# Performance work log

Measured on AMD Instinct MI355X. Metric: run time of the kernel, lower is better.

The kernel has to match this reference:

```python
import jax, jax.numpy as jnp
import numpy as np

N_NODES = 100000
N_EDGES = 1600000
N_FEAT = 128
HIDDEN = 128
N_CLASSES = 10
N_GRAPHS = 512


def setup_inputs() -> dict:
    key = jax.random.key(0)
    ks = jax.random.split(key, 20)

    def lin(k, fan_in, fan_out, bias=True):
        kw, kb = jax.random.split(k)
        s = 1.0 / np.sqrt(fan_in)
        W = jax.random.uniform(kw, (fan_in, fan_out), jnp.float32, -s, s)
        if bias:
            b = jax.random.uniform(kb, (fan_out,), jnp.float32, -s, s)
            return W, b
        return W

    x = jax.random.normal(ks[0], (N_NODES, N_FEAT), jnp.float32)
    edge_index = jax.random.randint(ks[1], (2, N_EDGES), 0, N_NODES)
    batch = jnp.sort(jax.random.randint(ks[2], (N_NODES,), 0, N_GRAPHS))

    w1l, b1 = lin(ks[3], N_FEAT, HIDDEN)
    w1r = lin(ks[4], N_FEAT, HIDDEN, bias=False)
    w2l, b2 = lin(ks[5], HIDDEN, HIDDEN)
    w2r = lin(ks[6], HIDDEN, HIDDEN, bias=False)
    w3l, b3 = lin(ks[7], HIDDEN, HIDDEN)
    w3r = lin(ks[8], HIDDEN, HIDDEN, bias=False)
    gate_w, gate_b = lin(ks[9], HIDDEN, 1)
    lin1_w, lin1_b = lin(ks[10], HIDDEN, HIDDEN)
    lin2_w, lin2_b = lin(ks[11], HIDDEN, N_CLASSES)

    return dict(x=x, edge_index=edge_index, batch=batch,
                w1l=w1l, b1=b1, w1r=w1r,
                w2l=w2l, b2=b2, w2r=w2r,
                w3l=w3l, b3=b3, w3r=w3r,
                gate_w=gate_w, gate_b=gate_b,
                lin1_w=lin1_w, lin1_b=lin1_b,
                lin2_w=lin2_w, lin2_b=lin2_b)


def _sage_conv(x, src, dst, Wl, bl, Wr, n_nodes):
    # PyG SAGEConv(mean): out = lin_l(mean_{j in N(i)} x_j) + lin_r(x_i)
    msg_sum = jax.ops.segment_sum(x[src], dst, num_segments=n_nodes)
    cnt = jax.ops.segment_sum(jnp.ones((src.shape[0], 1), x.dtype), dst,
                              num_segments=n_nodes)
    mean = msg_sum / jnp.maximum(cnt, 1.0)
    return mean @ Wl + bl + x @ Wr


def reference(x, edge_index, batch,
              w1l, b1, w1r, w2l, b2, w2r, w3l, b3, w3r,
              gate_w, gate_b, lin1_w, lin1_b, lin2_w, lin2_b):
    n = x.shape[0]
    src, dst = edge_index[0], edge_index[1]

    h = jax.nn.relu(_sage_conv(x, src, dst, w1l, b1, w1r, n))
    h = jax.nn.relu(_sage_conv(h, src, dst, w2l, b2, w2r, n))
    h = jax.nn.relu(_sage_conv(h, src, dst, w3l, b3, w3r, n))

    # AttentionalAggregation: scatter-softmax of gate over graph segments
    gate = h @ gate_w + gate_b                                  # [N, 1]
    m = jax.ops.segment_max(gate, batch, num_segments=N_GRAPHS)  # [G, 1]
    e = jnp.exp(gate - m[batch])
    s = jax.ops.segment_sum(e, batch, num_segments=N_GRAPHS)     # [G, 1]
    alpha = e / s[batch]
    pooled = jax.ops.segment_sum(alpha * h, batch, num_segments=N_GRAPHS)  # [G, H]

    out = jax.nn.relu(pooled @ lin1_w + lin1_b)
    # dropout is identity in eval mode
    out = out @ lin2_w + lin2_b
    return jax.nn.log_softmax(out, axis=-1)
```

## Files before the change

### kernel.cpp

```cpp
#include <hip/hip_runtime.h>
#include <stdint.h>

#define N_NODES 100000
#define N_EDGES 1600000
#define NF 128
#define NG 512
#define NC 10

#define NBUCK ((N_NODES + 255) / 256)
#define EPB 4096

#define KSTRIDE 136
#define GEMM_B ((N_NODES + 63) / 64)

#define CVT_B 6250
#define BT_B 384
#define BOUNDS_B 3
#define COUNT_B ((N_EDGES + EPB - 1) / EPB)

typedef short short8 __attribute__((ext_vector_type(8)));
typedef float f32x4 __attribute__((ext_vector_type(4)));

__device__ __forceinline__ unsigned short f2b(float f) {
    unsigned u = __float_as_uint(f);
    u += 0x7fffu + ((u >> 16) & 1u);
    return (unsigned short)(u >> 16);
}
__device__ __forceinline__ unsigned cvt2(float lo, float hi) {
    unsigned r;
    asm("v_cvt_pk_bf16_f32 %0, %1, %2" : "=v"(r) : "v"(lo), "v"(hi));
    return r;
}
__device__ __forceinline__ float lo16(unsigned v) { return __uint_as_float(v << 16); }
__device__ __forceinline__ float hi16(unsigned v) { return __uint_as_float(v & 0xffff0000u); }

__global__ __launch_bounds__(256) void prep_kernel(const float* __restrict__ x, unsigned short* __restrict__ xb,
                                                   const float* __restrict__ w1l, const float* __restrict__ w1r,
                                                   const float* __restrict__ w2l, const float* __restrict__ w2r,
                                                   const float* __restrict__ w3l, const float* __restrict__ w3r,
                                                   unsigned short* __restrict__ Bt,
                                                   const int* __restrict__ batch, int* __restrict__ gstart,
                                                   const int* __restrict__ dst, int* __restrict__ bcount) {
    const int b = blockIdx.x, t = threadIdx.x;
    if (b < CVT_B) {
        int i = b * 256 + t;
        const float4* ip = (const float4*)x;
        float4 a = ip[2 * i], c = ip[2 * i + 1];
        uint4 o;
        o.x = cvt2(a.x, a.y);
        o.y = cvt2(a.z, a.w);
        o.z = cvt2(c.x, c.y);
        o.w = cvt2(c.z, c.w);
        ((uint4*)xb)[i] = o;
    } else if (b < CVT_B + BT_B) {
        int i = (b - CVT_B) * 256 + t;
        int layer = i / (128 * 256);
        int r = i % (128 * 256);
        int n = r / 256, k = r % 256;
        const float* wl = (layer == 0) ? w1l : (layer == 1) ? w2l : w3l;
        const float* wr = (layer == 0) ? w1r : (layer == 1) ? w2r : w3r;
        float v = (k < 128) ? wl[k * 128 + n] : wr[(k - 128) * 128 + n];
        Bt[i] = f2b(v);
    } else if (b < CVT_B + BT_B + BOUNDS_B) {
        int g = (b - CVT_B - BT_B) * 256 + t;
        if (g > NG) return;
        int lo = 0, hi = N_NODES;
        while (lo < hi) {
            int mid = (lo + hi) >> 1;
            if (batch[mid] < g) lo = mid + 1; else hi = mid;
        }
        gstart[g] = lo;
    } else {
        __shared__ int h[NBUCK];
        for (int i = t; i < NBUCK; i += 256) h[i] = 0;
        __syncthreads();
        const int base = (b - CVT_B - BT_B - BOUNDS_B) * EPB;
        const int lim = min(base + EPB, N_EDGES);
        for (int i = base + t; i < lim; i += 256) atomicAdd(&h[dst[i] >> 8], 1);
        __syncthreads();
        for (int i = t; i < NBUCK; i += 256)
            if (h[i]) atomicAdd(&bcount[i], h[i]);
    }
}

__global__ __launch_bounds__(512) void bucket_scan(const int* __restrict__ bcount, int* __restrict__ bbase,
                                                   int* __restrict__ gcursor, int* __restrict__ rowptr) {
    __shared__ int sh[512];
    const int t = threadIdx.x;
    int v = (t < NBUCK) ? bcount[t] : 0;
    sh[t] = v;
    __syncthreads();
    for (int off = 1; off < 512; off <<= 1) {
        int u = (t >= off) ? sh[t - off] : 0;
        __syncthreads();
        sh[t] += u;
        __syncthreads();
    }
    if (t < NBUCK) {
        int e = sh[t] - v;
        bbase[t] = e;
        gcursor[t] = e;
    }
    if (t == NBUCK - 1) bbase[NBUCK] = sh[t];
    if (t == 0) rowptr[N_NODES] = N_EDGES;
}

__global__ __launch_bounds__(256) void bucket_scatter(const int* __restrict__ src, const int* __restrict__ dst,
                                                      int* __restrict__ gcursor, unsigned* __restrict__ brec) {
    __shared__ int h[NBUCK];
    for (int i = threadIdx.x; i < NBUCK; i += 256) h[i] = 0;
    __syncthreads();
    const int base = blockIdx.x * EPB;
    const int lim = min(base + EPB, N_EDGES);
    for (int i = base + threadIdx.x; i < lim; i += 256) atomicAdd(&h[dst[i] >> 8], 1);
    __syncthreads();
    for (int i = threadIdx.x; i < NBUCK; i += 256) {
        int c = h[i];
        if (c) h[i] = atomicAdd(&gcursor[i], c);
    }
    __syncthreads();
    for (int i = base + threadIdx.x; i < lim; i += 256) {
        int d = dst[i];
        int pos = atomicAdd(&h[d >> 8], 1);
        brec[pos] = ((unsigned)(d & 255) << 17) | (unsigned)src[i];
    }
}

__global__ __launch_bounds__(256) void bucket_fill(const unsigned* __restrict__ brec, const int* __restrict__ bbase,
                                                   int* __restrict__ rowptr, int* __restrict__ eidx) {
    __shared__ int nh[256];
    __shared__ int sc[256];
    const int b = blockIdx.x, t = threadIdx.x;
    const int beg = bbase[b], end = bbase[b + 1];
    nh[t] = 0;
    __syncthreads();
    for (int i = beg + t; i < end; i += 256) atomicAdd(&nh[brec[i] >> 17], 1);
    __syncthreads();
    int cnt = nh[t];
    sc[t] = cnt;
    __syncthreads();
    for (int off = 1; off < 256; off <<= 1) {
        int u = (t >= off) ? sc[t - off] : 0;
        __syncthreads();
        sc[t] += u;
        __syncthreads();
    }
    int excl = sc[t] - cnt;
    int node = b * 256 + t;
    if (node < N_NODES) rowptr[node] = beg + excl;
    nh[t] = beg + excl;
    __syncthreads();
    for (int i = beg + t; i < end; i += 256) {
        unsigned r = brec[i];
        int pos = atomicAdd(&nh[r >> 17], 1);
        eidx[pos] = (int)(r & 0x1FFFFu);
    }
}

__global__ __launch_bounds__(256) void agg_kernel(const unsigned short* __restrict__ F,
                                                  const int* __restrict__ rowptr,
                                                  const int* __restrict__ eidx,
                                                  unsigned short* __restrict__ M) {
    int node = blockIdx.x * 4 + (threadIdx.x >> 6);
    if (node >= N_NODES) return;
    const int lane = threadIdx.x & 63;
    const int quad = lane >> 4, ql = lane & 15;
    const int beg = rowptr[node], end = rowptr[node + 1];
    const char* Fb = (const char*)F;
    const unsigned qoff = (unsigned)ql << 4;

    float a0 = 0.f, a1 = 0.f, a2 = 0.f, a3 = 0.f, a4 = 0.f, a5 = 0.f, a6 = 0.f, a7 = 0.f;

    for (int cs = beg; cs < end; cs += 64) {
        int e = cs + lane;
        int idx = eidx[e < end ? e : end - 1];
        int n = end - cs;
        if (n > 64) n = 64;
        const int nfull = n >> 4;
        int l = quad;
        for (int g = 0; g < nfull; ++g, l += 16) {
            int r0 = __shfl(idx, l);
            int r1 = __shfl(idx, l + 4);
            int r2 = __shfl(idx, l + 8);
            int r3 = __shfl(idx, l + 12);
            uint4 v0 = *(const uint4*)(Fb + (((unsigned)r0 << 8) | qoff));
            uint4 v1 = *(const uint4*)(Fb + (((unsigned)r1 << 8) | qoff));
            uint4 v2 = *(const uint4*)(Fb + (((unsigned)r2 << 8) | qoff));
            uint4 v3 = *(const uint4*)(Fb + (((unsigned)r3 << 8) | qoff));
            a0 += lo16(v0.x) + lo16(v1.x) + lo16(v2.x) + lo16(v3.x);
            a1 += hi16(v0.x) + hi16(v1.x) + hi16(v2.x) + hi16(v3.x);
            a2 += lo16(v0.y) + lo16(v1.y) + lo16(v2.y) + lo16(v3.y);
            a3 += hi16(v0.y) + hi16(v1.y) + hi16(v2.y) + hi16(v3.y);
            a4 += lo16(v0.z) + lo16(v1.z) + lo16(v2.z) + lo16(v3.z);
            a5 += hi16(v0.z) + hi16(v1.z) + hi16(v2.z) + hi16(v3.z);
            a6 += lo16(v0.w) + lo16(v1.w) + lo16(v2.w) + lo16(v3.w);
            a7 += hi16(v0.w) + hi16(v1.w) + hi16(v2.w) + hi16(v3.w);
        }
        const int base = nfull << 4;
        for (int it = base; it < n; it += 4) {
            int l0 = it + quad;
            int r0 = __shfl(idx, l0 < n ? l0 : n - 1);
            float s0 = (l0 < n) ? 1.f : 0.f;
            uint4 v0 = *(const uint4*)(Fb + (((unsigned)r0 << 8) | qoff));
            a0 += s0 * lo16(v0.x); a1 += s0 * hi16(v0.x);
            a2 += s0 * lo16(v0.y); a3 += s0 * hi16(v0.y);
            a4 += s0 * lo16(v0.z); a5 += s0 * hi16(v0.z);
            a6 += s0 * lo16(v0.w); a7 += s0 * hi16(v0.w);
        }
    }

    a0 += __shfl_xor(a0, 16); a0 += __shfl_xor(a0, 32);
    a1 += __shfl_xor(a1, 16); a1 += __shfl_xor(a1, 32);
    a2 += __shfl_xor(a2, 16); a2 += __shfl_xor(a2, 32);
    a3 += __shfl_xor(a3, 16); a3 += __shfl_xor(a3, 32);
    a4 += __shfl_xor(a4, 16); a4 += __shfl_xor(a4, 32);
    a5 += __shfl_xor(a5, 16); a5 += __shfl_xor(a5, 32);
    a6 += __shfl_xor(a6, 16); a6 += __shfl_xor(a6, 32);
    a7 += __shfl_xor(a7, 16); a7 += __shfl_xor(a7, 32);

    if (quad == 0) {
        float inv = 1.0f / (float)max(end - beg, 1);
        uint4 o;
        o.x = cvt2(a0 * inv, a1 * inv);
        o.y = cvt2(a2 * inv, a3 * inv);
        o.z = cvt2(a4 * inv, a5 * inv);
        o.w = cvt2(a6 * inv, a7 * inv);
        ((uint4*)M)[(size_t)node * 16 + ql] = o;
    }
}

__global__ __launch_bounds__(256, 4) void gemm_kernel(const unsigned short* __restrict__ Am,
                                                      const unsigned short* __restrict__ Ax,
                                                      const unsigned short* __restrict__ Bt,
                                                      const float* __restrict__ bias,
                                                      unsigned short* __restrict__ Out,
                                                      const float* __restrict__ gatew,
                                                      const float* __restrict__ gateb,
                                                      float* __restrict__ gate) {
    const int t = threadIdx.x;
    const int wave = t >> 6, lane = t & 63;
    const int lrow = lane & 15, quad = lane >> 4;
    const int wrow0 = blockIdx.x * 64 + wave * 16;

    __shared__ __attribute__((aligned(16))) unsigned short Bs[128 * KSTRIDE];

    f32x4 acc[8];
#pragma unroll
    for (int j = 0; j < 8; ++j) acc[j] = (f32x4){0.f, 0.f, 0.f, 0.f};

    int arow = wrow0 + lrow;
    if (arow > N_NODES - 1) arow = N_NODES - 1;

    for (int p = 0; p < 2; ++p) {
        if (p) __syncthreads();
#pragma unroll
        for (int i = 0; i < 8; ++i) {
            int u = t + i * 256;
            int r = u >> 4, seg = u & 15;
            *(uint4*)(Bs + r * KSTRIDE + seg * 8) =
                *(const uint4*)(Bt + (size_t)r * 256 + p * 128 + seg * 8);
        }
        __syncthreads();

        const unsigned short* Aarr = p ? Ax : Am;
#pragma unroll
        for (int c = 0; c < 4; ++c) {
            const int kb = c * 32 + quad * 8;
            short8 af = *(const short8*)(Aarr + (size_t)arow * 128 + kb);
#pragma unroll
            for (int nt = 0; nt < 8; ++nt) {
                short8 bf = *(const short8*)(Bs + (nt * 16 + lrow) * KSTRIDE + kb);
                acc[nt] = __builtin_amdgcn_mfma_f32_16x16x32_bf16(af, bf, acc[nt], 0, 0, 0);
            }
        }
    }

    float gpart[4] = {0.f, 0.f, 0.f, 0.f};
    const int rbase = wrow0 + quad * 4;

#pragma unroll
    for (int nt = 0; nt < 8; ++nt) {
        int col = nt * 16 + lrow;
        float bc = bias[col];
        float gw = gatew ? gatew[col] : 0.f;
#pragma unroll
        for (int r = 0; r < 4; ++r) {
            int row = rbase + r;
            float v = fmaxf(acc[nt][r] + bc, 0.f);
            if (row < N_NODES) gpart[r] += v * gw;
            unsigned sv = (unsigned)f2b(v);
            unsigned nb = (unsigned)__shfl_xor((int)sv, 1);
            if (((lrow & 1) == 0) && row < N_NODES)
                *(unsigned*)(Out + (size_t)row * 128 + col) = sv | (nb << 16);
        }
    }
    if (gatew) {
        float gb = gateb[0];
#pragma unroll
        for (int r = 0; r < 4; ++r) {
            float g = gpart[r];
            g += __shfl_xor(g, 1);
            g += __shfl_xor(g, 2);
            g += __shfl_xor(g, 4);
            g += __shfl_xor(g, 8);
            if (lrow == 0) {
                int row = rbase + r;
                if (row < N_NODES) gate[row] = g + gb;
            }
        }
    }
}

__global__ __launch_bounds__(256) void pool_mlp_kernel(const unsigned short* __restrict__ h,
                                                       const float* __restrict__ gate,
                                                       const int* __restrict__ gstart,
                                                       const float* __restrict__ l1w,
                                                       const float* __restrict__ l1b,
                                                       const float* __restrict__ l2w,
                                                       const float* __restrict__ l2b,
                                                       float* __restrict__ out) {
    const int g = blockIdx.x;
    const int t = threadIdx.x;
    const int w = t >> 6, lane = t & 63;
    __shared__ float mred[4];
    __shared__ float sred[4];
    __shared__ float pax[4][128];
    __shared__ float pooled_s[128];
    __shared__ float hid_s[128];

    const int beg = gstart[g], end = gstart[g + 1];

    float m = -INFINITY;
    for (int i = beg + t; i < end; i += 256) m = fmaxf(m, gate[i]);
#pragma unroll
    for (int o = 32; o; o >>= 1) m = fmaxf(m, __shfl_xor(m, o));
    if (lane == 0) mred[w] = m;
    __syncthreads();
    m = fmaxf(fmaxf(mred[0], mred[1]), fmaxf(mred[2], mred[3]));

    float s = 0.f, ax = 0.f, ay = 0.f;
    const unsigned* hb = (const unsigned*)h;
    for (int i = beg + w; i < end; i += 4) {
        float e = expf(gate[i] - m);
        unsigned v = hb[(size_t)i * 64 + lane];
        s += e;
        ax += e * lo16(v);
        ay += e * hi16(v);
    }
    if (lane == 0) sred[w] = s;
    pax[w][2 * lane] = ax;
    pax[w][2 * lane + 1] = ay;
    __syncthreads();

    if (t < 128) {
        float ssum = sred[0] + sred[1] + sred[2] + sred[3];
        float invs = (ssum > 0.f) ? 1.0f / ssum : 0.f;
        pooled_s[t] = (pax[0][t] + pax[1][t] + pax[2][t] + pax[3][t]) * invs;
    }
    __syncthreads();

    if (w < 2) {
        const int o = w * 64 + lane;
        float acc = l1b[o];
        for (int k = 0; k < 128; ++k) acc += pooled_s[k] * l1w[k * 128 + o];
        hid_s[o] = fmaxf(acc, 0.f);
    }
    __syncthreads();

    if (w == 0) {
        float o10 = 0.f;
        if (lane < NC) {
            o10 = l2b[lane];
            for (int k = 0; k < 128; ++k) o10 += hid_s[k] * l2w[k * NC + lane];
        }
        float mm = -INFINITY;
#pragma unroll
        for (int j = 0; j < NC; ++j) mm = fmaxf(mm, __shfl(o10, j));
        float ss = 0.f;
#pragma unroll
        for (int j = 0; j < NC; ++j) ss += expf(__shfl(o10, j) - mm);
        float lse = mm + logf(ss);
        if (lane < NC) out[g * NC + lane] = o10 - lse;
    }
}

extern "C" void kernel_launch(void* const* d_in, const int* in_sizes, int n_in,
                              void* d_out, int out_size, void* d_ws, size_t ws_size,
                              hipStream_t stream) {
    const float* x   = (const float*)d_in[0];
    const int* ei    = (const int*)d_in[1];
    const int* batch = (const int*)d_in[2];
    const float* w1l = (const float*)d_in[3];
    const float* b1  = (const float*)d_in[4];
    const float* w1r = (const float*)d_in[5];
    const float* w2l = (const float*)d_in[6];
    const float* b2  = (const float*)d_in[7];
    const float* w2r = (const float*)d_in[8];
    const float* w3l = (const float*)d_in[9];
    const float* b3  = (const float*)d_in[10];
    const float* w3r = (const float*)d_in[11];
    const float* gw  = (const float*)d_in[12];
    const float* gb  = (const float*)d_in[13];
    const float* l1w = (const float*)d_in[14];
    const float* l1b = (const float*)d_in[15];
    const float* l2w = (const float*)d_in[16];
    const float* l2b = (const float*)d_in[17];
    float* out = (float*)d_out;

    const int* src = ei;
    const int* dst = ei + N_EDGES;

    char* base = (char*)d_ws;
    size_t off = 0;
    auto carve = [&](size_t bytes) -> void* {
        void* r = base + off;
        off = (off + bytes + 255) & ~(size_t)255;
        return r;
    };
    int* rowptr         = (int*)carve((size_t)(N_NODES + 1) * 4);
    int* eidx           = (int*)carve((size_t)N_EDGES * 4);
    unsigned short* Bt  = (unsigned short*)carve((size_t)3 * 128 * 256 * 2);
    unsigned short* xb  = (unsigned short*)carve((size_t)N_NODES * NF * 2);
    unsigned short* mn  = (unsigned short*)carve((size_t)N_NODES * NF * 2);
    unsigned short* hA  = (unsigned short*)carve((size_t)N_NODES * NF * 2);
    unsigned short* hB  = (unsigned short*)carve((size_t)N_NODES * NF * 2);
    float* gate         = (float*)carve((size_t)N_NODES * 4);
    int* gstart         = (int*)carve(513 * 4);
    int* bcount         = (int*)carve((NBUCK + 1) * 4);
    int* bbase          = (int*)carve((NBUCK + 1) * 4);
    int* gcursor        = (int*)carve((NBUCK + 1) * 4);
    unsigned* brec      = (unsigned*)mn;

    hipMemsetAsync(bcount, 0, (size_t)NBUCK * 4, stream);

    prep_kernel<<<CVT_B + BT_B + BOUNDS_B + COUNT_B, 256, 0, stream>>>(
        x, xb, w1l, w1r, w2l, w2r, w3l, w3r, Bt, batch, gstart, dst, bcount);

    bucket_scan<<<1, 512, 0, stream>>>(bcount, bbase, gcursor, rowptr);
    bucket_scatter<<<COUNT_B, 256, 0, stream>>>(src, dst, gcursor, brec);
    bucket_fill<<<NBUCK, 256, 0, stream>>>(brec, bbase, rowptr, eidx);

    const int AGG_B = (N_NODES + 3) / 4;

    agg_kernel<<<AGG_B, 256, 0, stream>>>(xb, rowptr, eidx, mn);
    gemm_kernel<<<GEMM_B, 256, 0, stream>>>(mn, xb, Bt, b1, hA, nullptr, nullptr, nullptr);
    agg_kernel<<<AGG_B, 256, 0, stream>>>(hA, rowptr, eidx, mn);
    gemm_kernel<<<GEMM_B, 256, 0, stream>>>(mn, hA, Bt + 32768, b2, hB, nullptr, nullptr, nullptr);
    agg_kernel<<<AGG_B, 256, 0, stream>>>(hB, rowptr, eidx, mn);
    gemm_kernel<<<GEMM_B, 256, 0, stream>>>(mn, hB, Bt + 65536, b3, hA, gw, gb, gate);

    pool_mlp_kernel<<<NG, 256, 0, stream>>>(hA, gate, gstart, l1w, l1b, l2w, l2b, out);
}
```

Baseline: 439.2 us.

## Fuse CSR build kernels into one cooperative kernel; prefetch GEMM A fragments

```diff
diff --git a/kernel.cpp b/kernel.cpp
--- a/kernel.cpp
+++ b/kernel.cpp
@@ -1,5 +1,8 @@
 #include <hip/hip_runtime.h>
+#include <hip/hip_cooperative_groups.h>
 #include <stdint.h>
+
+namespace cg = cooperative_groups;
 
 #define N_NODES 100000
 #define N_EDGES 1600000
@@ -83,77 +86,81 @@
     }
 }
 
-__global__ __launch_bounds__(512) void bucket_scan(const int* __restrict__ bcount, int* __restrict__ bbase,
-                                                   int* __restrict__ gcursor, int* __restrict__ rowptr) {
-    __shared__ int sh[512];
-    const int t = threadIdx.x;
-    int v = (t < NBUCK) ? bcount[t] : 0;
-    sh[t] = v;
-    __syncthreads();
-    for (int off = 1; off < 512; off <<= 1) {
-        int u = (t >= off) ? sh[t - off] : 0;
-        __syncthreads();
-        sh[t] += u;
-        __syncthreads();
-    }
-    if (t < NBUCK) {
-        int e = sh[t] - v;
-        bbase[t] = e;
-        gcursor[t] = e;
-    }
-    if (t == NBUCK - 1) bbase[NBUCK] = sh[t];
-    if (t == 0) rowptr[N_NODES] = N_EDGES;
-}
-
-__global__ __launch_bounds__(256) void bucket_scatter(const int* __restrict__ src, const int* __restrict__ dst,
-                                                      int* __restrict__ gcursor, unsigned* __restrict__ brec) {
-    __shared__ int h[NBUCK];
-    for (int i = threadIdx.x; i < NBUCK; i += 256) h[i] = 0;
-    __syncthreads();
-    const int base = blockIdx.x * EPB;
-    const int lim = min(base + EPB, N_EDGES);
-    for (int i = base + threadIdx.x; i < lim; i += 256) atomicAdd(&h[dst[i] >> 8], 1);
-    __syncthreads();
-    for (int i = threadIdx.x; i < NBUCK; i += 256) {
-        int c = h[i];
-        if (c) h[i] = atomicAdd(&gcursor[i], c);
-    }
-    __syncthreads();
-    for (int i = base + threadIdx.x; i < lim; i += 256) {
-        int d = dst[i];
-        int pos = atomicAdd(&h[d >> 8], 1);
-        brec[pos] = ((unsigned)(d & 255) << 17) | (unsigned)src[i];
-    }
-}
-
-__global__ __launch_bounds__(256) void bucket_fill(const unsigned* __restrict__ brec, const int* __restrict__ bbase,
-                                                   int* __restrict__ rowptr, int* __restrict__ eidx) {
-    __shared__ int nh[256];
-    __shared__ int sc[256];
+__global__ __launch_bounds__(256) void csr_kernel(const int* __restrict__ src, const int* __restrict__ dst,
+                                                  const int* __restrict__ bcount, int* __restrict__ bbase,
+                                                  int* __restrict__ gcursor, int* __restrict__ rowptr,
+                                                  unsigned* __restrict__ brec, int* __restrict__ eidx) {
+    cg::grid_group grid = cg::this_grid();
+    __shared__ int sA[512];
+    __shared__ int sB[512];
     const int b = blockIdx.x, t = threadIdx.x;
-    const int beg = bbase[b], end = bbase[b + 1];
-    nh[t] = 0;
-    __syncthreads();
-    for (int i = beg + t; i < end; i += 256) atomicAdd(&nh[brec[i] >> 17], 1);
-    __syncthreads();
-    int cnt = nh[t];
-    sc[t] = cnt;
-    __syncthreads();
-    for (int off = 1; off < 256; off <<= 1) {
-        int u = (t >= off) ? sc[t - off] : 0;
-        __syncthreads();
-        sc[t] += u;
-        __syncthreads();
-    }
-    int excl = sc[t] - cnt;
-    int node = b * 256 + t;
-    if (node < N_NODES) rowptr[node] = beg + excl;
-    nh[t] = beg + excl;
-    __syncthreads();
-    for (int i = beg + t; i < end; i += 256) {
-        unsigned r = brec[i];
-        int pos = atomicAdd(&nh[r >> 17], 1);
-        eidx[pos] = (int)(r & 0x1FFFFu);
+
+    if (b == 0) {
+        sA[t] = (t < NBUCK) ? bcount[t] : 0;
+        sA[t + 256] = (t + 256 < NBUCK) ? bcount[t + 256] : 0;
+        __syncthreads();
+        int* pin = sA;
+        int* pout = sB;
+        for (int off = 1; off < 512; off <<= 1) {
+            for (int j = t; j < 512; j += 256)
+                pout[j] = pin[j] + (j >= off ? pin[j - off] : 0);
+            __syncthreads();
+            int* tmp = pin; pin = pout; pout = tmp;
+        }
+        for (int j = t; j < NBUCK; j += 256) {
+            int e = pin[j] - bcount[j];
+            bbase[j] = e;
+            gcursor[j] = e;
+        }
+        if (t == 0) { bbase[NBUCK] = N_EDGES; rowptr[N_NODES] = N_EDGES; }
+    }
+    grid.sync();
+
+    {
+        for (int i = t; i < NBUCK; i += 256) sA[i] = 0;
+        __syncthreads();
+        const int base = b * EPB;
+        const int lim = min(base + EPB, N_EDGES);
+        for (int i = base + t; i < lim; i += 256) atomicAdd(&sA[dst[i] >> 8], 1);
+        __syncthreads();
+        for (int i = t; i < NBUCK; i += 256) {
+            int c = sA[i];
+            if (c) sA[i] = atomicAdd(&gcursor[i], c);
+        }
+        __syncthreads();
+        for (int i = base + t; i < lim; i += 256) {
+            int d = dst[i];
+            int pos = atomicAdd(&sA[d >> 8], 1);
+            brec[pos] = ((unsigned)(d & 255) << 17) | (unsigned)src[i];
+        }
+    }
+    grid.sync();
+
+    {
+        const int beg = bbase[b], end = bbase[b + 1];
+        sA[t] = 0;
+        __syncthreads();
+        for (int i = beg + t; i < end; i += 256) atomicAdd(&sA[brec[i] >> 17], 1);
+        __syncthreads();
+        int cnt = sA[t];
+        sB[t] = cnt;
+        __syncthreads();
+        for (int off = 1; off < 256; off <<= 1) {
+            int u = (t >= off) ? sB[t - off] : 0;
+            __syncthreads();
+            sB[t] += u;
+            __syncthreads();
+        }
+        int excl = sB[t] - cnt;
+        int node = b * 256 + t;
+        if (node < N_NODES) rowptr[node] = beg + excl;
+        sA[t] = beg + excl;
+        __syncthreads();
+        for (int i = beg + t; i < end; i += 256) {
+            unsigned r = brec[i];
+            int pos = atomicAdd(&sA[r >> 17], 1);
+            eidx[pos] = (int)(r & 0x1FFFFu);
+        }
     }
 }
 
@@ -251,6 +258,15 @@
     int arow = wrow0 + lrow;
     if (arow > N_NODES - 1) arow = N_NODES - 1;
 
+    short8 afm[4], afx[4];
+#pragma unroll
+    for (int c = 0; c < 4; ++c) {
+        const int kb = c * 32 + quad * 8;
+        afm[c] = *(const short8*)(Am + (size_t)arow * 128 + kb);
+        afx[c] = *(const short8*)(Ax + (size_t)arow * 128 + kb);
+    }
+
+#pragma unroll
     for (int p = 0; p < 2; ++p) {
         if (p) __syncthreads();
 #pragma unroll
@@ -262,11 +278,10 @@
         }
         __syncthreads();
 
-        const unsigned short* Aarr = p ? Ax : Am;
 #pragma unroll
         for (int c = 0; c < 4; ++c) {
             const int kb = c * 32 + quad * 8;
-            short8 af = *(const short8*)(Aarr + (size_t)arow * 128 + kb);
+            short8 af = p ? afx[c] : afm[c];
 #pragma unroll
             for (int nt = 0; nt < 8; ++nt) {
                 short8 bf = *(const short8*)(Bs + (nt * 16 + lrow) * KSTRIDE + kb);
@@ -436,9 +451,12 @@
     prep_kernel<<<CVT_B + BT_B + BOUNDS_B + COUNT_B, 256, 0, stream>>>(
         x, xb, w1l, w1r, w2l, w2r, w3l, w3r, Bt, batch, gstart, dst, bcount);
 
-    bucket_scan<<<1, 512, 0, stream>>>(bcount, bbase, gcursor, rowptr);
-    bucket_scatter<<<COUNT_B, 256, 0, stream>>>(src, dst, gcursor, brec);
-    bucket_fill<<<NBUCK, 256, 0, stream>>>(brec, bbase, rowptr, eidx);
+    {
+        void* cargs[] = {(void*)&src, (void*)&dst, (void*)&bcount, (void*)&bbase,
+                         (void*)&gcursor, (void*)&rowptr, (void*)&brec, (void*)&eidx};
+        hipLaunchCooperativeKernel((const void*)csr_kernel, dim3(COUNT_B), dim3(256),
+                                   cargs, 0, stream);
+    }
 
     const int AGG_B = (N_NODES + 3) / 4;
 
```

Result: slower. 569.6 us (+29.7%).
